# Kernel tuning notes

Hardware: AMD Instinct MI355X
Metric: run time of the kernel (lower is better)

The kernel has to match this reference:

```python
import jax, jax.numpy as jnp
import numpy as np

RADII = (0.8, 1.6)
NSAMPLES = (16, 32)
NUM_GRIDPOINTS = 216


def rotate_z(points, theta):
    # points (b, n, m, 3), theta (b, n); rotate xy about z-axis
    c = jnp.cos(theta)[:, :, None]
    s = jnp.sin(theta)[:, :, None]
    x, y, z = points[..., 0], points[..., 1], points[..., 2]
    return jnp.stack([c * x - s * y, s * x + c * y, z], axis=-1)


def ball_query(d2, radius, nsample):
    # d2: (b, Ng, K) squared distances. Returns first nsample in-radius point
    # indices per query (CUDA ball_query semantics: pad with first found index,
    # 0 if none found).
    K = d2.shape[-1]
    ar = jnp.arange(K, dtype=jnp.int32)
    scores = jnp.where(d2 < radius * radius, ar, K)  # K == sentinel for 'not in ball'
    idx = -jax.lax.top_k(-scores, nsample)[0]        # nsample smallest => first hits, ascending
    first = idx[..., :1]
    idx = jnp.where(idx >= K, first, idx)
    idx = jnp.where(idx >= K, 0, idx)
    return idx


def gather_group(xyz, feats_t, new_xyz, idx):
    # xyz (b,K,3), feats_t (b,K,C), new_xyz (b,Ng,3), idx (b,Ng,ns)
    gx = jax.vmap(lambda p, i: p[i])(xyz, idx)      # (b,Ng,ns,3)
    gf = jax.vmap(lambda f, i: f[i])(feats_t, idx)  # (b,Ng,ns,C)
    rel = gx - new_xyz[:, :, None, :]               # use_xyz=True relative coords
    return jnp.concatenate([rel, gf], axis=-1)      # (b,Ng,ns,3+C)


def setup_inputs() -> dict:
    key = jax.random.key(0)
    ks = jax.random.split(key, 12)
    b, n, m, K, C = 2, 48, NUM_GRIDPOINTS, 2048, 128
    proposals = jax.random.uniform(ks[0], (b, n, 7), dtype=jnp.float32)
    keypoint_xyz = jax.random.normal(ks[1], (b, K, 3), dtype=jnp.float32)
    keypoint_features = jax.random.normal(ks[2], (b, C, K), dtype=jnp.float32)
    grid_noise = jax.random.uniform(ks[3], (b, n, m, 3), dtype=jnp.float32)

    def lin(k, o, i):
        return jax.random.normal(k, (o, i), dtype=jnp.float32) / np.float32(np.sqrt(i))

    w0_0 = lin(ks[4], 64, C + 3)
    w0_1 = lin(ks[5], 64, 64)
    w1_0 = lin(ks[6], 64, C + 3)
    w1_1 = lin(ks[7], 64, 64)
    red_w0 = lin(ks[8], 256, 128 * m)
    red_w1 = lin(ks[9], 256, 256)
    z64 = jnp.zeros((64,), jnp.float32)
    return {
        'proposals': proposals, 'keypoint_xyz': keypoint_xyz,
        'keypoint_features': keypoint_features, 'grid_noise': grid_noise,
        'w0_0': w0_0, 'b0_0': z64, 'w0_1': w0_1, 'b0_1': z64,
        'w1_0': w1_0, 'b1_0': z64, 'w1_1': w1_1, 'b1_1': z64,
        'red_w0': red_w0, 'red_b0': jnp.zeros((256,), jnp.float32),
        'red_w1': red_w1, 'red_b1': jnp.zeros((256,), jnp.float32),
    }


def reference(proposals, keypoint_xyz, keypoint_features, grid_noise,
              w0_0, b0_0, w0_1, b0_1, w1_0, b1_0, w1_1, b1_1,
              red_w0, red_b0, red_w1, red_b1):
    b, n, _ = proposals.shape
    m = NUM_GRIDPOINTS
    # sample_gridpoints: uniform in box dims, rotate by yaw, shift to center
    grid = grid_noise * proposals[:, :, None, 3:6]
    grid = rotate_z(grid, proposals[..., 6]) + proposals[:, :, None, 0:3]
    new_xyz = grid.reshape(b, n * m, 3)                      # (b, Ng, 3)
    # squared pairwise distances via |a|^2 + |b|^2 - 2ab (avoids (b,Ng,K,3) temp)
    d2 = (jnp.sum(new_xyz * new_xyz, -1)[:, :, None]
          + jnp.sum(keypoint_xyz * keypoint_xyz, -1)[:, None, :]
          - 2.0 * jnp.einsum('bnd,bkd->bnk', new_xyz, keypoint_xyz))
    feats_t = jnp.transpose(keypoint_features, (0, 2, 1))    # (b, K, C)
    scale_params = [((w0_0, b0_0), (w0_1, b0_1)), ((w1_0, b1_0), (w1_1, b1_1))]
    outs = []
    for radius, ns, layers in zip(RADII, NSAMPLES, scale_params):
        idx = ball_query(d2, radius, ns)                     # (b, Ng, ns)
        x = gather_group(keypoint_xyz, feats_t, new_xyz, idx)  # (b, Ng, ns, 3+C)
        for W, bias in layers:                               # shared 1x1-conv MLP (BN folded)
            x = jax.nn.relu(jnp.einsum('bnsc,oc->bnso', x, W) + bias)
        outs.append(jnp.max(x, axis=2))                      # max-pool over neighbors
    x = jnp.concatenate(outs, axis=-1)                       # (b, Ng, Cout)
    Cout = x.shape[-1]
    # (b, Cout, n, m).permute(0,2,1,3).view(b, n, Cout*m) equivalent
    x = x.reshape(b, n, m, Cout).transpose(0, 1, 3, 2).reshape(b, n, Cout * m)
    x = jax.nn.relu(x @ red_w0.T + red_b0)
    x = jax.nn.relu(x @ red_w1.T + red_b1)
    return x
```

## Files before the change

### kernel.cpp

```cpp
#include <hip/hip_runtime.h>
#include <cstdint>

#define NPROP  48
#define MGRID  216
#define NPT    (NPROP*MGRID)
#define KPT    2048
#define CFEAT  128
#define R0SQ   0.64f
#define R1SQ   2.56f
#define NS0    16
#define NS1    32
#define KRED   (CFEAT*MGRID)
#define NPOINTS (2*NPT)
#define NKSPLIT 108

typedef float f32x4  __attribute__((ext_vector_type(4)));
typedef short bf16x8 __attribute__((ext_vector_type(8)));
typedef unsigned long long ull;

#define AFRAG_OFF 0
#define KX4_OFF   8192
#define Q0_OFF    24576
#define POOL_OFF  548864
#define PT_OFF    3203072
#define PART_OFF  5857280

__device__ __forceinline__ unsigned short bf_rne(float x) {
    unsigned u = __float_as_uint(x);
    return (unsigned short)((u + 0x7fffu + ((u >> 16) & 1u)) >> 16);
}
__device__ __forceinline__ float bf_f32(unsigned short h) {
    return __uint_as_float(((unsigned)h) << 16);
}

__global__ __launch_bounds__(64) void k_pre(
    const float* __restrict__ kxyz,
    const float* __restrict__ w01, const float* __restrict__ w11,
    float* __restrict__ ws)
{
    int bid = blockIdx.x;
    if (bid < 16) {
        int kc = bid & 1, ot = (bid >> 1) & 3, s = bid >> 3;
        const float* W = s ? w11 : w01;
        int l   = threadIdx.x;
        int row = ot*16 + (l & 15);
        int k0  = kc*32 + (l >> 4)*8;
        union { unsigned short u16[8]; bf16x8 v; } hh, hl;
#pragma unroll
        for (int j = 0; j < 8; ++j) {
            float x  = W[row*64 + k0 + j];
            unsigned short hi = bf_rne(x);
            hh.u16[j] = hi;
            hl.u16[j] = bf_rne(x - bf_f32(hi));
        }
        bf16x8* Whi = (bf16x8*)(ws + AFRAG_OFF);
        bf16x8* Wlo = Whi + 16*64;
        int fi = (s*4 + ot)*2 + kc;
        Whi[fi*64 + l] = hh.v;
        Wlo[fi*64 + l] = hl.v;
    } else {
        int idx = (bid - 16)*64 + threadIdx.x;
        const float* kp = kxyz + (size_t)idx*3;
        float kx = kp[0], ky = kp[1], kz = kp[2];
        float kn2 = fmaf(kz, kz, fmaf(ky, ky, kx*kx));
        f32x4 v = {kx, ky, kz, kn2};
        ((f32x4*)(ws + KX4_OFF))[idx] = v;
    }
}

__global__ __launch_bounds__(256) void k_qproj(
    const float* __restrict__ kxyz, const float* __restrict__ feats,
    const float* __restrict__ w0, const float* __restrict__ b0,
    const float* __restrict__ w1, const float* __restrict__ b1,
    float* __restrict__ ws)
{
    __shared__ float wl[64*131];
    int bid  = blockIdx.x;
    int kgrp = bid & 511;
    int s    = (bid >> 9) & 1;
    int b    = bid >> 10;
    const float* W    = s ? w1 : w0;
    const float* bias = s ? b1 : b0;
    for (int i = threadIdx.x; i < 64*131; i += 256) wl[i] = W[i];
    __syncthreads();
    int k = kgrp*4 + (threadIdx.x >> 6);
    int o = threadIdx.x & 63;
    float acc = bias[o];
    const float* kp = kxyz + ((size_t)b*KPT + k)*3;
    acc = fmaf(wl[o*131+0], kp[0], acc);
    acc = fmaf(wl[o*131+1], kp[1], acc);
    acc = fmaf(wl[o*131+2], kp[2], acc);
    const float* f = feats + (size_t)b*CFEAT*KPT + k;
#pragma unroll 8
    for (int c = 0; c < CFEAT; ++c)
        acc = fmaf(wl[o*131+3+c], f[(size_t)c*KPT], acc);
    ws[Q0_OFF + (size_t)s*(2*KPT*64) + ((size_t)b*KPT + k)*64 + o] = acc;
}

template <int NST>
__device__ __forceinline__ void build_hfrag(
    const float* __restrict__ Qb, const int* __restrict__ idxl,
    const float* __restrict__ u_lds,
    bf16x8 (&Hhi)[NST][2], bf16x8 (&Hlo)[NST][2], int lane)
{
    const int g = lane >> 4;
#pragma unroll
    for (int st = 0; st < NST; ++st) {
        int sp = idxl[st*16 + (lane & 15)];
        const float* qr = Qb + ((size_t)sp << 6) + g*8;
#pragma unroll
        for (int kc = 0; kc < 2; ++kc) {
            f32x4 q0 = *(const f32x4*)(qr + kc*32);
            f32x4 q1 = *(const f32x4*)(qr + kc*32 + 4);
            f32x4 u0 = *(const f32x4*)(u_lds + kc*32 + g*8);
            f32x4 u1 = *(const f32x4*)(u_lds + kc*32 + g*8 + 4);
            union { unsigned short u16[8]; bf16x8 v; } hh, hl;
#pragma unroll
            for (int j = 0; j < 4; ++j) {
                float x = fmaxf(q0[j] - u0[j], 0.f);
                unsigned short hi = bf_rne(x);
                hh.u16[j] = hi;
                hl.u16[j] = bf_rne(x - bf_f32(hi));
                float y = fmaxf(q1[j] - u1[j], 0.f);
                unsigned short hi2 = bf_rne(y);
                hh.u16[j+4] = hi2;
                hl.u16[j+4] = bf_rne(y - bf_f32(hi2));
            }
            Hhi[st][kc] = hh.v;
            Hlo[st][kc] = hl.v;
        }
    }
}

template <int NST>
__device__ __forceinline__ float eval_T(
    const bf16x8* Whi, const bf16x8* Wlo,
    const float* __restrict__ bs,
    const bf16x8 (&Hhi)[NST][2], const bf16x8 (&Hlo)[NST][2],
    int sbase, int lane)
{
    float r0, r1, r2, r3;
#define EVAL_OT(OT, ROUT)                                                     \
    {                                                                         \
        int fi = (sbase + (OT))*2;                                            \
        bf16x8 wh0 = Whi[(fi+0)*64 + lane];                                   \
        bf16x8 wh1 = Whi[(fi+1)*64 + lane];                                   \
        bf16x8 wl0 = Wlo[(fi+0)*64 + lane];                                   \
        bf16x8 wl1 = Wlo[(fi+1)*64 + lane];                                   \
        float bc = bs[(OT)*16 + (lane & 15)];                                 \
        f32x4 rmax = {0.f, 0.f, 0.f, 0.f};                                    \
        _Pragma("unroll")                                                     \
        for (int st = 0; st < NST; ++st) {                                    \
            f32x4 acc = {0.f, 0.f, 0.f, 0.f};                                 \
            acc = __builtin_amdgcn_mfma_f32_16x16x32_bf16(Hlo[st][0], wh0, acc, 0,0,0); \
            acc = __builtin_amdgcn_mfma_f32_16x16x32_bf16(Hlo[st][1], wh1, acc, 0,0,0); \
            acc = __builtin_amdgcn_mfma_f32_16x16x32_bf16(Hhi[st][0], wl0, acc, 0,0,0); \
            acc = __builtin_amdgcn_mfma_f32_16x16x32_bf16(Hhi[st][1], wl1, acc, 0,0,0); \
            acc = __builtin_amdgcn_mfma_f32_16x16x32_bf16(Hhi[st][0], wh0, acc, 0,0,0); \
            acc = __builtin_amdgcn_mfma_f32_16x16x32_bf16(Hhi[st][1], wh1, acc, 0,0,0); \
            _Pragma("unroll")                                                 \
            for (int r = 0; r < 4; ++r)                                       \
                rmax[r] = fmaxf(rmax[r], fmaxf(acc[r] + bc, 0.f));            \
        }                                                                     \
        float mm = fmaxf(fmaxf(rmax[0], rmax[1]), fmaxf(rmax[2], rmax[3]));   \
        mm = fmaxf(mm, __shfl_xor(mm, 16));                                   \
        mm = fmaxf(mm, __shfl_xor(mm, 32));                                   \
        ROUT = mm;                                                            \
    }
    EVAL_OT(0, r0) EVAL_OT(1, r1) EVAL_OT(2, r2) EVAL_OT(3, r3)
#undef EVAL_OT
    float v01 = (lane & 16) ? r1 : r0;
    float v23 = (lane & 16) ? r3 : r2;
    return (lane & 32) ? v23 : v01;
}

__global__ __launch_bounds__(512, 4) void k_main(
    const float* __restrict__ proposals, const float* __restrict__ grid_noise,
    const float* __restrict__ w00, const float* __restrict__ b01,
    const float* __restrict__ w10, const float* __restrict__ b11,
    float* __restrict__ ws)
{
    __shared__ __align__(16) float afrag[8192];
    __shared__ int idx0s[8][NS0];
    __shared__ int idx1s[8][NS1];
    __shared__ __align__(16) float u0l[8][64], u1l[8][64];
    const int wid  = threadIdx.x >> 6;
    const int lane = threadIdx.x & 63;

    {
        const f32x4* src = (const f32x4*)(ws + AFRAG_OFF);
        f32x4* dst = (f32x4*)afrag;
        for (int t = threadIdx.x; t < 2048; t += 512) dst[t] = src[t];
    }
    __syncthreads();

    const int p = blockIdx.x*8 + wid;
    int b   = p / NPT;
    int rem = p - b*NPT;
    int i   = rem / MGRID;
    int g   = rem - i*MGRID;

    float a0x = w00[lane*131+0], a0y = w00[lane*131+1], a0z = w00[lane*131+2];
    float a1x = w10[lane*131+0], a1y = w10[lane*131+1], a1z = w10[lane*131+2];

    const float* pr = proposals  + ((size_t)b*NPROP + i)*7;
    const float* gn = grid_noise + (((size_t)b*NPROP + i)*MGRID + g)*3;
    float gx = gn[0]*pr[3], gy = gn[1]*pr[4], gz = gn[2]*pr[5];
    float th = pr[6];
    float ss = sinf(th), cc = cosf(th);
    float nx = cc*gx - ss*gy + pr[0];
    float ny = ss*gx + cc*gy + pr[1];
    float nz = gz + pr[2];
    float pn2 = nx*nx + ny*ny + nz*nz;
    u0l[wid][lane] = a0x*nx + a0y*ny + a0z*nz;
    u1l[wid][lane] = a1x*nx + a1y*ny + a1z*nz;

    int* idx0 = idx0s[wid];
    int* idx1 = idx1s[wid];
    int cnt0 = 0, cnt1 = 0;
    const f32x4* kx4 = (const f32x4*)(ws + KX4_OFF) + (size_t)b*KPT;
    ull ltm = (1ull << lane) - 1ull;

#define BQ_PROC(D2, RSQ, KK, CNT, IDX, NSV)                                   \
    {                                                                         \
        ull m = __ballot((D2) < RSQ);                                         \
        if (m) {                                                              \
            int pre = __popcll(m & ltm);                                      \
            if (((m >> lane) & 1ull) && CNT + pre < NSV) IDX[CNT + pre] = (KK);\
            CNT += __popcll(m);                                               \
        }                                                                     \
    }

    for (int ck = 0; ck < KPT/64; ck += 2) {
        f32x4 ka  = kx4[ck*64 + lane];
        f32x4 kc2 = kx4[ck*64 + 64 + lane];
        float dta = fmaf(nz, ka.z, fmaf(ny, ka.y, nx*ka.x));
        float d2a = fmaf(-2.f, dta, pn2 + ka.w);
        float dtb = fmaf(nz, kc2.z, fmaf(ny, kc2.y, nx*kc2.x));
        float d2b = fmaf(-2.f, dtb, pn2 + kc2.w);
        int kka = ck*64 + lane, kkb = kka + 64;
        if (cnt0 < NS0) {
            BQ_PROC(d2a, R0SQ, kka, cnt0, idx0, NS0)
            BQ_PROC(d2b, R0SQ, kkb, cnt0, idx0, NS0)
        }
        if (cnt1 < NS1) {
            BQ_PROC(d2a, R1SQ, kka, cnt1, idx1, NS1)
            BQ_PROC(d2b, R1SQ, kkb, cnt1, idx1, NS1)
        }
        if (cnt0 >= NS0 && cnt1 >= NS1) break;
    }
#undef BQ_PROC

    if (lane == 0) {
        if (cnt0 == 0) idx0[0] = 0;
        if (cnt1 == 0) idx1[0] = 0;
    }
    asm volatile("s_waitcnt lgkmcnt(0)" ::: "memory");
    __builtin_amdgcn_wave_barrier();
    int na0 = cnt0 ? min(cnt0, NS0) : 1;
    int na1 = cnt1 ? min(cnt1, NS1) : 1;
    int f0 = idx0[0], f1 = idx1[0];
    if (lane >= na0 && lane < NS0) idx0[lane] = f0;
    if (lane >= na1 && lane < NS1) idx1[lane] = f1;
    asm volatile("s_waitcnt lgkmcnt(0)" ::: "memory");
    __builtin_amdgcn_wave_barrier();

    const float*  Qb0 = ws + Q0_OFF + (size_t)b*(KPT*64);
    const float*  Qb1 = ws + Q0_OFF + (size_t)(2*KPT*64) + (size_t)b*(KPT*64);
    const bf16x8* Whi = (const bf16x8*)afrag;
    const bf16x8* Wlo = Whi + 16*64;

    bf16x8 H0hi[1][2], H0lo[1][2], H1hi[2][2], H1lo[2][2];
    build_hfrag<1>(Qb0, idx0, u0l[wid], H0hi, H0lo, lane);
    build_hfrag<2>(Qb1, idx1, u1l[wid], H1hi, H1lo, lane);

    float mx0 = eval_T<1>(Whi, Wlo, b01, H0hi, H0lo, 0, lane);
    float mx1 = eval_T<2>(Whi, Wlo, b11, H1hi, H1lo, 4, lane);

    ws[POOL_OFF + (size_t)p*CFEAT + lane]      = mx0;
    ws[POOL_OFF + (size_t)p*CFEAT + 64 + lane] = mx1;
}

template <int W>
__device__ __forceinline__ void ptr_tile(const float* __restrict__ in,
                                         float* __restrict__ out,
                                         float* __restrict__ t, int g0)
{
    for (int idx = threadIdx.x; idx < 128*W; idx += 256) {
        int gg = idx >> 7, c = idx & 127;
        t[c*(W+1) + gg] = in[(size_t)(g0+gg)*128 + c];
    }
    __syncthreads();
    for (int idx = threadIdx.x; idx < 128*W; idx += 256) {
        int c = idx / W, gg = idx - c*W;
        out[c*216 + g0 + gg] = t[c*(W+1) + gg];
    }
}

__global__ __launch_bounds__(256) void k_ptr(float* __restrict__ ws)
{
    __shared__ float t[128*33];
    int bid = blockIdx.x;
    int row = bid / 7, tt = bid - row*7;
    const float* in = ws + POOL_OFF + (size_t)row*MGRID*CFEAT;
    float* out = ws + PT_OFF + (size_t)row*KRED;
    if (tt < 6) ptr_tile<32>(in, out, t, tt*32);
    else        ptr_tile<24>(in, out, t, 192);
}

__global__ __launch_bounds__(256) void k_red0(
    const float* __restrict__ A, const float* __restrict__ w0,
    float* __restrict__ part)
{
    __shared__ __align__(16) float Al[96*68];
    __shared__ __align__(16) float Bl[64*68];
    int bid = blockIdx.x;
    int ot  = bid & 3;
    int ks  = bid >> 2;
    int tid = threadIdx.x;
    int tx  = tid & 15, ty = tid >> 4;
    float acc[6][4] = {};

    for (int chunk = 0; chunk < 4; ++chunk) {
        int kk0 = ks*256 + chunk*64;
#pragma unroll
        for (int j = 0; j < 6; ++j) {
            int f4i = tid + j*256;
            int rr = f4i >> 4, c4 = f4i & 15;
            float4 v = *(const float4*)(A + (size_t)rr*KRED + kk0 + c4*4);
            *(float4*)(Al + rr*68 + c4*4) = v;
        }
#pragma unroll
        for (int j = 0; j < 4; ++j) {
            int f4i = tid + j*256;
            int rr = f4i >> 4, c4 = f4i & 15;
            float4 v = *(const float4*)(w0 + (size_t)(ot*64+rr)*KRED + kk0 + c4*4);
            *(float4*)(Bl + rr*68 + c4*4) = v;
        }
        __syncthreads();
#pragma unroll
        for (int k4 = 0; k4 < 16; ++k4) {
            float4 av[6], bv[4];
#pragma unroll
            for (int q = 0; q < 6; ++q) av[q] = *(const float4*)(Al + (ty*6+q)*68 + k4*4);
#pragma unroll
            for (int u = 0; u < 4; ++u) bv[u] = *(const float4*)(Bl + (u*16+tx)*68 + k4*4);
#pragma unroll
            for (int q = 0; q < 6; ++q)
#pragma unroll
                for (int u = 0; u < 4; ++u) {
                    acc[q][u] = fmaf(av[q].x, bv[u].x, acc[q][u]);
                    acc[q][u] = fmaf(av[q].y, bv[u].y, acc[q][u]);
                    acc[q][u] = fmaf(av[q].z, bv[u].z, acc[q][u]);
                    acc[q][u] = fmaf(av[q].w, bv[u].w, acc[q][u]);
                }
        }
        __syncthreads();
    }
    float* pp = part + (size_t)ks*(96*256);
#pragma unroll
    for (int q = 0; q < 6; ++q)
#pragma unroll
        for (int u = 0; u < 4; ++u)
            pp[(size_t)(ty*6+q)*256 + ot*64 + u*16 + tx] = acc[q][u];
}

__global__ __launch_bounds__(256) void k_fin(
    const float* __restrict__ part, const float* __restrict__ rb0,
    const float* __restrict__ w1, const float* __restrict__ rb1,
    float* __restrict__ out)
{
    __shared__ __align__(16) float hbuf[256];
    int r = blockIdx.x, o = threadIdx.x;
    const float* pp = part + (size_t)r*256 + o;
    float s0 = 0.f, s1 = 0.f, s2 = 0.f, s3 = 0.f;
#pragma unroll 4
    for (int ks = 0; ks < NKSPLIT; ks += 4) {
        s0 += pp[(size_t)(ks+0)*(96*256)];
        s1 += pp[(size_t)(ks+1)*(96*256)];
        s2 += pp[(size_t)(ks+2)*(96*256)];
        s3 += pp[(size_t)(ks+3)*(96*256)];
    }
    float h = fmaxf(((s0 + s1) + (s2 + s3)) + rb0[o], 0.f);
    hbuf[o] = h;
    __syncthreads();
    float a0 = rb1[o], a1 = 0.f, a2 = 0.f, a3 = 0.f;
    const float4* wrow = (const float4*)(w1 + (size_t)o*256);
    const float4* hv   = (const float4*)hbuf;
#pragma unroll 8
    for (int j = 0; j < 64; ++j) {
        float4 w = wrow[j], x = hv[j];
        a0 = fmaf(w.x, x.x, a0);
        a1 = fmaf(w.y, x.y, a1);
        a2 = fmaf(w.z, x.z, a2);
        a3 = fmaf(w.w, x.w, a3);
    }
    out[(size_t)r*256 + o] = fmaxf((a0 + a1) + (a2 + a3), 0.f);
}

extern "C" void kernel_launch(void* const* d_in, const int* in_sizes, int n_in,
                              void* d_out, int out_size, void* d_ws, size_t ws_size,
                              hipStream_t stream)
{
    (void)in_sizes; (void)n_in; (void)out_size; (void)ws_size;
    const float* proposals = (const float*)d_in[0];
    const float* kxyz      = (const float*)d_in[1];
    const float* feats     = (const float*)d_in[2];
    const float* gnoise    = (const float*)d_in[3];
    const float* w0_0 = (const float*)d_in[4];
    const float* b0_0 = (const float*)d_in[5];
    const float* w0_1 = (const float*)d_in[6];
    const float* b0_1 = (const float*)d_in[7];
    const float* w1_0 = (const float*)d_in[8];
    const float* b1_0 = (const float*)d_in[9];
    const float* w1_1 = (const float*)d_in[10];
    const float* b1_1 = (const float*)d_in[11];
    const float* rw0  = (const float*)d_in[12];
    const float* rb0  = (const float*)d_in[13];
    const float* rw1  = (const float*)d_in[14];
    const float* rb1  = (const float*)d_in[15];
    float* ws  = (float*)d_ws;
    float* out = (float*)d_out;

    k_pre  <<<  80,  64, 0, stream>>>(kxyz, w0_1, w1_1, ws);
    k_qproj<<<2048, 256, 0, stream>>>(kxyz, feats, w0_0, b0_0, w1_0, b1_0, ws);
    k_main <<<2592, 512, 0, stream>>>(proposals, gnoise,
                                      w0_0, b0_1, w1_0, b1_1, ws);
    k_ptr  <<< 672, 256, 0, stream>>>(ws);
    k_red0 <<< 432, 256, 0, stream>>>(ws + PT_OFF, rw0, ws + PART_OFF);
    k_fin  <<<  96, 256, 0, stream>>>(ws + PART_OFF, rb0, rw1, rb1, out);
}
```

Baseline: 231.1 us.

## Merge prep kernels, use hardware bf16 convert, split MFMA accumulator chains

Merges the weight-fragment/keypoint prep kernel and the query projection kernel into one launch, removing one kernel launch and its serialization gap. Swaps the manual round-to-nearest-even bf16 conversion in fragment building for the HIP library conversion, which may lower to a hardware convert instruction. Splits each six-MFMA dependent chain into two independent accumulators that are summed at the end, shortening the dependency chain. The summation order changes slightly, which can perturb low-order bits.

```diff
diff --git a/kernel.cpp b/kernel.cpp
--- a/kernel.cpp
+++ b/kernel.cpp
@@ -1,4 +1,5 @@
 #include <hip/hip_runtime.h>
+#include <hip/hip_bf16.h>
 #include <cstdint>
 
 #define NPROP  48
@@ -32,17 +33,26 @@
 __device__ __forceinline__ float bf_f32(unsigned short h) {
     return __uint_as_float(((unsigned)h) << 16);
 }
-
-__global__ __launch_bounds__(64) void k_pre(
-    const float* __restrict__ kxyz,
+__device__ __forceinline__ unsigned short bf_cvt(float x) {
+    union { __hip_bfloat16 h; unsigned short u; } c;
+    c.h = __float2bfloat16(x);
+    return c.u;
+}
+
+__global__ __launch_bounds__(256) void k_prep(
+    const float* __restrict__ kxyz, const float* __restrict__ feats,
+    const float* __restrict__ w00, const float* __restrict__ b00,
+    const float* __restrict__ w10, const float* __restrict__ b10,
     const float* __restrict__ w01, const float* __restrict__ w11,
     float* __restrict__ ws)
 {
+    __shared__ float shmem[64*131];
     int bid = blockIdx.x;
-    if (bid < 16) {
-        int kc = bid & 1, ot = (bid >> 1) & 3, s = bid >> 3;
+    if (bid < 4) {
+        int sub = threadIdx.x >> 6, l = threadIdx.x & 63;
+        int fid = bid*4 + sub;
+        int kc = fid & 1, ot = (fid >> 1) & 3, s = fid >> 3;
         const float* W = s ? w11 : w01;
-        int l   = threadIdx.x;
         int row = ot*16 + (l & 15);
         int k0  = kc*32 + (l >> 4)*8;
         union { unsigned short u16[8]; bf16x8 v; } hh, hl;
@@ -58,43 +68,35 @@
         int fi = (s*4 + ot)*2 + kc;
         Whi[fi*64 + l] = hh.v;
         Wlo[fi*64 + l] = hl.v;
-    } else {
-        int idx = (bid - 16)*64 + threadIdx.x;
+    } else if (bid < 20) {
+        int idx = (bid - 4)*256 + threadIdx.x;
         const float* kp = kxyz + (size_t)idx*3;
         float kx = kp[0], ky = kp[1], kz = kp[2];
         float kn2 = fmaf(kz, kz, fmaf(ky, ky, kx*kx));
         f32x4 v = {kx, ky, kz, kn2};
         ((f32x4*)(ws + KX4_OFF))[idx] = v;
-    }
-}
-
-__global__ __launch_bounds__(256) void k_qproj(
-    const float* __restrict__ kxyz, const float* __restrict__ feats,
-    const float* __restrict__ w0, const float* __restrict__ b0,
-    const float* __restrict__ w1, const float* __restrict__ b1,
-    float* __restrict__ ws)
-{
-    __shared__ float wl[64*131];
-    int bid  = blockIdx.x;
-    int kgrp = bid & 511;
-    int s    = (bid >> 9) & 1;
-    int b    = bid >> 10;
-    const float* W    = s ? w1 : w0;
-    const float* bias = s ? b1 : b0;
-    for (int i = threadIdx.x; i < 64*131; i += 256) wl[i] = W[i];
-    __syncthreads();
-    int k = kgrp*4 + (threadIdx.x >> 6);
-    int o = threadIdx.x & 63;
-    float acc = bias[o];
-    const float* kp = kxyz + ((size_t)b*KPT + k)*3;
-    acc = fmaf(wl[o*131+0], kp[0], acc);
-    acc = fmaf(wl[o*131+1], kp[1], acc);
-    acc = fmaf(wl[o*131+2], kp[2], acc);
-    const float* f = feats + (size_t)b*CFEAT*KPT + k;
+    } else {
+        int qb   = bid - 20;
+        int kgrp = qb & 511;
+        int s    = (qb >> 9) & 1;
+        int b    = qb >> 10;
+        const float* W    = s ? w10 : w00;
+        const float* bias = s ? b10 : b00;
+        for (int i = threadIdx.x; i < 64*131; i += 256) shmem[i] = W[i];
+        __syncthreads();
+        int k = kgrp*4 + (threadIdx.x >> 6);
+        int o = threadIdx.x & 63;
+        float acc = bias[o];
+        const float* kp = kxyz + ((size_t)b*KPT + k)*3;
+        acc = fmaf(shmem[o*131+0], kp[0], acc);
+        acc = fmaf(shmem[o*131+1], kp[1], acc);
+        acc = fmaf(shmem[o*131+2], kp[2], acc);
+        const float* f = feats + (size_t)b*CFEAT*KPT + k;
 #pragma unroll 8
-    for (int c = 0; c < CFEAT; ++c)
-        acc = fmaf(wl[o*131+3+c], f[(size_t)c*KPT], acc);
-    ws[Q0_OFF + (size_t)s*(2*KPT*64) + ((size_t)b*KPT + k)*64 + o] = acc;
+        for (int c = 0; c < CFEAT; ++c)
+            acc = fmaf(shmem[o*131+3+c], f[(size_t)c*KPT], acc);
+        ws[Q0_OFF + (size_t)s*(2*KPT*64) + ((size_t)b*KPT + k)*64 + o] = acc;
+    }
 }
 
 template <int NST>
@@ -118,13 +120,13 @@
 #pragma unroll
             for (int j = 0; j < 4; ++j) {
                 float x = fmaxf(q0[j] - u0[j], 0.f);
-                unsigned short hi = bf_rne(x);
+                unsigned short hi = bf_cvt(x);
                 hh.u16[j] = hi;
-                hl.u16[j] = bf_rne(x - bf_f32(hi));
+                hl.u16[j] = bf_cvt(x - bf_f32(hi));
                 float y = fmaxf(q1[j] - u1[j], 0.f);
-                unsigned short hi2 = bf_rne(y);
+                unsigned short hi2 = bf_cvt(y);
                 hh.u16[j+4] = hi2;
-                hl.u16[j+4] = bf_rne(y - bf_f32(hi2));
+                hl.u16[j+4] = bf_cvt(y - bf_f32(hi2));
             }
             Hhi[st][kc] = hh.v;
             Hlo[st][kc] = hl.v;
@@ -151,16 +153,17 @@
         f32x4 rmax = {0.f, 0.f, 0.f, 0.f};                                    \
         _Pragma("unroll")                                                     \
         for (int st = 0; st < NST; ++st) {                                    \
-            f32x4 acc = {0.f, 0.f, 0.f, 0.f};                                 \
-            acc = __builtin_amdgcn_mfma_f32_16x16x32_bf16(Hlo[st][0], wh0, acc, 0,0,0); \
-            acc = __builtin_amdgcn_mfma_f32_16x16x32_bf16(Hlo[st][1], wh1, acc, 0,0,0); \
-            acc = __builtin_amdgcn_mfma_f32_16x16x32_bf16(Hhi[st][0], wl0, acc, 0,0,0); \
-            acc = __builtin_amdgcn_mfma_f32_16x16x32_bf16(Hhi[st][1], wl1, acc, 0,0,0); \
-            acc = __builtin_amdgcn_mfma_f32_16x16x32_bf16(Hhi[st][0], wh0, acc, 0,0,0); \
-            acc = __builtin_amdgcn_mfma_f32_16x16x32_bf16(Hhi[st][1], wh1, acc, 0,0,0); \
+            f32x4 accA = {0.f, 0.f, 0.f, 0.f};                                \
+            f32x4 accB = {0.f, 0.f, 0.f, 0.f};                                \
+            accA = __builtin_amdgcn_mfma_f32_16x16x32_bf16(Hlo[st][0], wh0, accA, 0,0,0); \
+            accB = __builtin_amdgcn_mfma_f32_16x16x32_bf16(Hlo[st][1], wh1, accB, 0,0,0); \
+            accA = __builtin_amdgcn_mfma_f32_16x16x32_bf16(Hhi[st][0], wl0, accA, 0,0,0); \
+            accB = __builtin_amdgcn_mfma_f32_16x16x32_bf16(Hhi[st][1], wl1, accB, 0,0,0); \
+            accA = __builtin_amdgcn_mfma_f32_16x16x32_bf16(Hhi[st][0], wh0, accA, 0,0,0); \
+            accB = __builtin_amdgcn_mfma_f32_16x16x32_bf16(Hhi[st][1], wh1, accB, 0,0,0); \
             _Pragma("unroll")                                                 \
             for (int r = 0; r < 4; ++r)                                       \
-                rmax[r] = fmaxf(rmax[r], fmaxf(acc[r] + bc, 0.f));            \
+                rmax[r] = fmaxf(rmax[r], fmaxf((accA[r] + accB[r]) + bc, 0.f)); \
         }                                                                     \
         float mm = fmaxf(fmaxf(rmax[0], rmax[1]), fmaxf(rmax[2], rmax[3]));   \
         mm = fmaxf(mm, __shfl_xor(mm, 16));                                   \
@@ -422,8 +425,8 @@
     float* ws  = (float*)d_ws;
     float* out = (float*)d_out;
 
-    k_pre  <<<  80,  64, 0, stream>>>(kxyz, w0_1, w1_1, ws);
-    k_qproj<<<2048, 256, 0, stream>>>(kxyz, feats, w0_0, b0_0, w1_0, b1_0, ws);
+    k_prep <<<2068, 256, 0, stream>>>(kxyz, feats, w0_0, b0_0, w1_0, b1_0,
+                                      w0_1, w1_1, ws);
     k_main <<<2592, 512, 0, stream>>>(proposals, gnoise,
                                       w0_0, b0_1, w1_0, b1_1, ws);
     k_ptr  <<< 672, 256, 0, stream>>>(ws);
```

Result: no change. 229.6 us (-0.7%).
